# Kernel optimization log

Hardware: AMD Instinct MI355X
Metric: run time of the kernel (lower is better)

Reference implementation:

```python
import jax, jax.numpy as jnp
import numpy as np

N = 4096
IN_SIZE = 512
MLP_W = 16
HID = 512
MID = 64  # hardcoded tgc2 output size in the torch module
OUT = 128
BN_EPS = 1e-5


def setup_inputs() -> dict:
    key = jax.random.key(0)
    ks = jax.random.split(key, 24)
    adj = (jax.random.uniform(ks[0], (N, N)) < 0.05).astype(jnp.float32)
    xdeg = jax.random.uniform(ks[1], (N, N), dtype=jnp.float32)
    ydeg = jax.random.uniform(ks[2], (N, N), dtype=jnp.float32)
    u = lambda k, sh, fan: jax.random.uniform(k, sh, jnp.float32, -1.0, 1.0) / np.sqrt(fan)
    return {
        "adj": adj, "xdeg": xdeg, "ydeg": ydeg,
        # edge MLP: 3 -> MLP_W -> 2
        "mlp_w1": u(ks[3], (3, MLP_W), 3), "mlp_b1": jnp.zeros((MLP_W,), jnp.float32),
        "mlp_w2": u(ks[4], (MLP_W, 2), MLP_W), "mlp_b2": jnp.zeros((2,), jnp.float32),
        # positional linear: Linear(N, in_size) applied to eye(N) -> pe = W^T + b
        "pe_w": u(ks[5], (N, IN_SIZE), N), "pe_b": jnp.zeros((IN_SIZE,), jnp.float32),
        # GCN weights
        "gc1_w": u(ks[6], (IN_SIZE, HID), HID),
        "lin2_w": u(ks[7], (HID, MID), HID), "lin2_b": jnp.zeros((MID,), jnp.float32),
        "gc3_w": u(ks[8], (MID, OUT), OUT),
        # BatchNorm (eval mode: running stats)
        "bn1_g": jnp.ones((HID,), jnp.float32), "bn1_b": jnp.zeros((HID,), jnp.float32),
        "bn1_m": jnp.zeros((HID,), jnp.float32), "bn1_v": jnp.ones((HID,), jnp.float32),
        "bn2_g": jnp.ones((OUT,), jnp.float32), "bn2_b": jnp.zeros((OUT,), jnp.float32),
        "bn2_m": jnp.zeros((OUT,), jnp.float32), "bn2_v": jnp.ones((OUT,), jnp.float32),
    }


def reference(adj, xdeg, ydeg, mlp_w1, mlp_b1, mlp_w2, mlp_b2, pe_w, pe_b,
              gc1_w, lin2_w, lin2_b, gc3_w,
              bn1_g, bn1_b, bn1_m, bn1_v, bn2_g, bn2_b, bn2_m, bn2_v):
    # Edge MLP + softmax over [adj, xdeg, ydeg] features; torch only computes it
    # at nonzero adj entries then scatters into a dense mask. Since the mask is
    # multiplied by adj, computing densely and multiplying is exactly equivalent.
    feats = jnp.stack([adj, xdeg, ydeg], axis=-1)          # [N, N, 3]
    h = jax.nn.relu(jnp.einsum('nmf,fw->nmw', feats, mlp_w1) + mlp_b1)
    logits = jnp.einsum('nmw,wc->nmc', h, mlp_w2) + mlp_b2  # [N, N, 2]
    mask = jax.nn.softmax(logits, axis=-1)[..., 1]          # [N, N]
    a = adj * mask + jnp.eye(adj.shape[0], dtype=adj.dtype)

    # Degree normalization: A' = D_row^{-1/2} A D_col^{-1/2} (broadcast, no diag matmuls)
    rowsum = jnp.sum(a, axis=1)
    colsum = jnp.sum(a, axis=0)
    d_row = jnp.where(rowsum > 0, rowsum ** -0.5, 0.0)
    d_col = jnp.where(colsum > 0, colsum ** -0.5, 0.0)
    a = d_row[:, None] * a * d_col[None, :]

    # pe = Linear(eye(N)) = W^T + b (eval mode, dropout off)
    pe = pe_w + pe_b[None, :]                               # [N, IN_SIZE]

    h = a @ (pe @ gc1_w)                                    # GCN layer 1
    h = (h - bn1_m) * (bn1_g / jnp.sqrt(bn1_v + BN_EPS)) + bn1_b
    h = h @ lin2_w + lin2_b                                 # tgc2
    mid = h
    h = jax.nn.relu(h)
    h = a @ (h @ gc3_w)                                     # GCN layer 3
    out = (h - bn2_m) * (bn2_g / jnp.sqrt(bn2_v + BN_EPS)) + bn2_b
    return out, mid
```

## Files before the change

### kernel.cpp

```cpp
#include <hip/hip_runtime.h>
#include <hip/hip_bf16.h>

#define NN 4096
#define INS 512
#define HIDW 512
#define MIDW 64
#define OUTW 128
#define CAP 384
#define SEG 96
#define BN_EPS 1e-5f
#define CS_BLOCKS 256
#define CS_ROWS (NN / CS_BLOCKS)
#define NSTRIP 8

__global__ __launch_bounds__(256) void k_count(
    const float* __restrict__ adj,
    unsigned long long* __restrict__ msk, int* __restrict__ cnt,
    int* __restrict__ dflag)
{
    const int t = threadIdx.x;
    const int wave = t >> 6, lane = t & 63;
    const int gw = blockIdx.x * 4 + wave;
    const int i = gw >> 3, s = gw & 7;
    const int colbase = s * 512;
    const float* __restrict__ base = adj + (size_t)i * NN + colbase + 4 * lane;
    float4 a4a = *reinterpret_cast<const float4*>(base);
    float4 a4b = *reinterpret_cast<const float4*>(base + 256);
    const float av[8] = {a4a.x, a4a.y, a4a.z, a4a.w,
                         a4b.x, a4b.y, a4b.z, a4b.w};
    unsigned long long m[8];
    int total = 0;
    #pragma unroll
    for (int c = 0; c < 8; ++c) {
        int col = colbase + ((c < 4) ? (4 * lane + c) : (256 + 4 * lane + c - 4));
        bool diag = (col == i);
        bool act = (av[c] != 0.f) || diag;
        if (diag) dflag[i] = (av[c] != 0.f) ? 1 : 0;
        m[c] = __ballot(act);
        total += __popcll(m[c]);
    }
    if (lane == 0) {
        unsigned long long* mp = msk + (size_t)gw * 8;
        #pragma unroll
        for (int c = 0; c < 8; ++c) mp[c] = m[c];
        cnt[gw] = total;
    }
}

__global__ __launch_bounds__(256) void k_prefix(
    const int* __restrict__ cnt, int* __restrict__ off, int* __restrict__ nnz)
{
    int i = blockIdx.x * 256 + threadIdx.x;
    int run = 0;
    #pragma unroll
    for (int s = 0; s < NSTRIP; ++s) {
        off[i * NSTRIP + s] = run;
        run += cnt[i * NSTRIP + s];
    }
    nnz[i] = (run < CAP) ? run : CAP;
}

__global__ __launch_bounds__(256) void k_fill(
    const float* __restrict__ xdeg, const float* __restrict__ ydeg,
    const unsigned long long* __restrict__ msk, const int* __restrict__ off,
    const int* __restrict__ dflag,
    const float* __restrict__ w1, const float* __restrict__ b1,
    const float* __restrict__ w2, const float* __restrict__ b2,
    float* __restrict__ a_vals, int* __restrict__ a_cols,
    float* __restrict__ rs_part)
{
    __shared__ float shb[16], sw1x[16], sw1y[16], sw2[32], sb2[2];
    __shared__ int   scol[4][SEG];
    __shared__ float sx[4][SEG];
    __shared__ float sy[4][SEG];
    const int t = threadIdx.x;
    const int wave = t >> 6, lane = t & 63;
    if (t < 16) {
        shb[t]  = b1[t] + w1[t];
        sw1x[t] = w1[16 + t];
        sw1y[t] = w1[32 + t];
    }
    if (t < 32) sw2[t] = w2[t];
    if (t < 2)  sb2[t] = b2[t];
    __syncthreads();

    const int gw = __builtin_amdgcn_readfirstlane(blockIdx.x * 4 + wave);
    const int i = gw >> 3, s = gw & 7;
    const int colbase = s * 512;
    const size_t rbase = (size_t)i * NN + colbase + 4 * lane;
    float4 x4a = *reinterpret_cast<const float4*>(xdeg + rbase);
    float4 x4b = *reinterpret_cast<const float4*>(xdeg + rbase + 256);
    float4 y4a = *reinterpret_cast<const float4*>(ydeg + rbase);
    float4 y4b = *reinterpret_cast<const float4*>(ydeg + rbase + 256);
    const unsigned long long* __restrict__ mp = msk + (size_t)gw * 8;
    unsigned long long mm[8];
    #pragma unroll
    for (int c = 0; c < 8; ++c) mm[c] = mp[c];
    const int wb = off[gw];
    const int hasde = dflag[i];

    int bases[8];
    bases[0] = 0;
    #pragma unroll
    for (int c = 1; c < 8; ++c) bases[c] = bases[c - 1] + __popcll(mm[c - 1]);
    const int cnt_ = bases[7] + __popcll(mm[7]);
    const int n = (cnt_ < SEG) ? cnt_ : SEG;
    const unsigned long long lt = (1ULL << lane) - 1ULL;

    const float xv[8] = {x4a.x, x4a.y, x4a.z, x4a.w,
                         x4b.x, x4b.y, x4b.z, x4b.w};
    const float yv[8] = {y4a.x, y4a.y, y4a.z, y4a.w,
                         y4b.x, y4b.y, y4b.z, y4b.w};
    #pragma unroll
    for (int c = 0; c < 8; ++c) {
        if ((mm[c] >> lane) & 1ULL) {
            int pos = bases[c] + __popcll(mm[c] & lt);
            if (pos < SEG) {
                scol[wave][pos] = colbase + ((c < 4) ? (4 * lane + c)
                                                     : (256 + 4 * lane + c - 4));
                sx[wave][pos] = xv[c];
                sy[wave][pos] = yv[c];
            }
        }
    }

    float* __restrict__ gv = a_vals + (size_t)i * CAP;
    int*   __restrict__ gc = a_cols + (size_t)i * CAP;
    float local = 0.f;
    for (int p = lane; p < n; p += 64) {
        int col = scol[wave][p];
        float x = sx[wave][p], y = sy[wave][p];
        float l0 = sb2[0], l1 = sb2[1];
        #pragma unroll
        for (int w = 0; w < 16; ++w) {
            float hw = fmaf(x, sw1x[w], shb[w]);
            hw = fmaf(y, sw1y[w], hw);
            hw = fmaxf(hw, 0.f);
            l0 = fmaf(hw, sw2[2 * w],     l0);
            l1 = fmaf(hw, sw2[2 * w + 1], l1);
        }
        float v = 1.f / (1.f + __expf(l0 - l1));
        if (col == i) v = hasde ? (v + 1.f) : 1.f;
        int gp = wb + p;
        if (gp < CAP) { gc[gp] = col; gv[gp] = v; }
        local += v;
    }
    #pragma unroll
    for (int o = 32; o >= 1; o >>= 1)
        local += __shfl_down(local, o, 64);
    if (lane == 0) rs_part[gw] = local;
}

__global__ __launch_bounds__(256) void k_colsum(
    const float* __restrict__ a_vals, const int* __restrict__ a_cols,
    const int* __restrict__ nnz, float* __restrict__ P)
{
    __shared__ float ls[NN];
    const int t = threadIdx.x;
    const int b = blockIdx.x;
    for (int j = t; j < NN; j += 256) ls[j] = 0.f;
    __syncthreads();
    const int r0 = b * CS_ROWS;
    for (int r = r0; r < r0 + CS_ROWS; ++r) {
        const int n = nnz[r];
        const float* __restrict__ vr = a_vals + (size_t)r * CAP;
        const int*   __restrict__ cr = a_cols + (size_t)r * CAP;
        for (int p = t; p < n; p += 256)
            atomicAdd(&ls[cr[p]], vr[p]);
    }
    __syncthreads();
    for (int j = t; j < NN; j += 256)
        P[(size_t)b * NN + j] = ls[j];
}

__global__ __launch_bounds__(512) void k_misc(
    const float* __restrict__ lin2_w, const float* __restrict__ lin2_b,
    const float* __restrict__ bn1_g, const float* __restrict__ bn1_b,
    const float* __restrict__ bn1_m, const float* __restrict__ bn1_v,
    const float* __restrict__ bn2_g, const float* __restrict__ bn2_b,
    const float* __restrict__ bn2_m, const float* __restrict__ bn2_v,
    const float* __restrict__ rs_part, const float* __restrict__ P,
    float* __restrict__ Wp, float* __restrict__ c1,
    float* __restrict__ s2g, float* __restrict__ t2g,
    float* __restrict__ d_row, float* __restrict__ d_col)
{
    const int t = threadIdx.x;
    if (blockIdx.x == 0) {
        __shared__ float t1s[HIDW];
        {
            int h = t;
            float s1 = bn1_g[h] * rsqrtf(bn1_v[h] + BN_EPS);
            t1s[h] = bn1_b[h] - bn1_m[h] * s1;
            for (int m = 0; m < MIDW; ++m)
                Wp[(size_t)h * MIDW + m] = s1 * lin2_w[(size_t)h * MIDW + m];
        }
        __syncthreads();
        if (t < MIDW) {
            float acc = lin2_b[t];
            for (int h = 0; h < HIDW; ++h)
                acc = fmaf(t1s[h], lin2_w[(size_t)h * MIDW + t], acc);
            c1[t] = acc;
        } else if (t >= 64 && t < 64 + OUTW) {
            int j = t - 64;
            float s2 = bn2_g[j] * rsqrtf(bn2_v[j] + BN_EPS);
            s2g[j] = s2;
            t2g[j] = bn2_b[j] - bn2_m[j] * s2;
        }
    } else {
        int j = (blockIdx.x - 1) * 512 + t;
        float r = 0.f;
        #pragma unroll
        for (int s = 0; s < NSTRIP; ++s) r += rs_part[j * NSTRIP + s];
        d_row[j] = (r > 0.f) ? 1.f / sqrtf(r) : 0.f;
        float c = 0.f;
        for (int b = 0; b < CS_BLOCKS; ++b)
            c += P[(size_t)b * NN + j];
        d_col[j] = (c > 0.f) ? 1.f / sqrtf(c) : 0.f;
    }
}

template <bool ABIAS, bool ROWSCALE>
__global__ __launch_bounds__(256) void k_thin(
    const float* __restrict__ A, const float* __restrict__ B,
    const float* __restrict__ abias, const float* __restrict__ rscale,
    float* __restrict__ C, int M, int K)
{
    __shared__ float As[64][36];
    __shared__ float Bs[64][64];
    const int t = threadIdx.x;
    const int bm = blockIdx.x * 32;
    const int c2 = t & 31, rg = t >> 5;

    float acc[4][2] = {};

    for (int k0 = 0; k0 < K; k0 += 64) {
        #pragma unroll
        for (int l = 0; l < 8; ++l) {
            int e = t + l * 256;
            int r = e >> 6, k = e & 63;
            float v = A[(size_t)(bm + r) * K + k0 + k];
            if (ABIAS) v += abias[k0 + k];
            As[k][r] = v;
        }
        #pragma unroll
        for (int l = 0; l < 16; ++l) {
            int e = t + l * 256;
            int k = e >> 6, n = e & 63;
            Bs[k][n] = B[(size_t)(k0 + k) * 64 + n];
        }
        __syncthreads();
        #pragma unroll
        for (int k = 0; k < 64; ++k) {
            float4 a4 = *reinterpret_cast<const float4*>(&As[k][rg * 4]);
            float2 b2 = *reinterpret_cast<const float2*>(&Bs[k][2 * c2]);
            acc[0][0] = fmaf(a4.x, b2.x, acc[0][0]);
            acc[0][1] = fmaf(a4.x, b2.y, acc[0][1]);
            acc[1][0] = fmaf(a4.y, b2.x, acc[1][0]);
            acc[1][1] = fmaf(a4.y, b2.y, acc[1][1]);
            acc[2][0] = fmaf(a4.z, b2.x, acc[2][0]);
            acc[2][1] = fmaf(a4.z, b2.y, acc[2][1]);
            acc[3][0] = fmaf(a4.w, b2.x, acc[3][0]);
            acc[3][1] = fmaf(a4.w, b2.y, acc[3][1]);
        }
        __syncthreads();
    }

    #pragma unroll
    for (int u = 0; u < 4; ++u) {
        int r = bm + rg * 4 + u;
        float sc = ROWSCALE ? rscale[r] : 1.f;
        float2 o = make_float2(acc[u][0] * sc, acc[u][1] * sc);
        *reinterpret_cast<float2*>(&C[(size_t)r * 64 + 2 * c2]) = o;
    }
}

template <bool WITH_MID>
__global__ __launch_bounds__(256) void k_spmm(
    const float* __restrict__ a_vals, const int* __restrict__ a_cols,
    const int* __restrict__ nnz, const float* __restrict__ X,
    const float* __restrict__ d_row, const float* __restrict__ d_col,
    const float* __restrict__ c1,
    float* __restrict__ O1, float* __restrict__ O2)
{
    __shared__ float sv[2][CAP];
    __shared__ int   scl[2][CAP];
    __shared__ float sacc[4][64];
    const int t = threadIdx.x;
    const int wave = t >> 6, lane = t & 63;
    const int rb = wave >> 1, h = wave & 1;
    const int i = blockIdx.x * 2 + rb;
    const int n = nnz[i];
    const int n16 = (n + 15) & ~15;
    const float* __restrict__ vrow = a_vals + (size_t)i * CAP;
    const int*   __restrict__ crow = a_cols + (size_t)i * CAP;

    for (int p = h * 64 + lane; p < n16; p += 128) {
        bool ok = p < n;
        sv[rb][p]  = ok ? vrow[p] : 0.f;
        scl[rb][p] = ok ? crow[p] : 0;
    }
    __syncthreads();

    const int eh = lane >> 5;
    const int lc = lane & 31;
    const int Q  = n16 >> 1;
    const int Qh = Q >> 1;

    float a0 = 0.f, a1 = 0.f;
    for (int q = h * Qh; q < (h + 1) * Qh; q += 4) {
        #pragma unroll
        for (int j = 0; j < 4; ++j) {
            int p = 2 * (q + j) + eh;
            float v = sv[rb][p];
            int c = scl[rb][p];
            float2 x = *reinterpret_cast<const float2*>(X + (size_t)c * 64 + 2 * lc);
            a0 = fmaf(v, x.x, a0);
            a1 = fmaf(v, x.y, a1);
        }
    }
    a0 += __shfl_xor(a0, 32);
    a1 += __shfl_xor(a1, 32);
    if (lane < 32) { sacc[wave][2 * lc] = a0; sacc[wave][2 * lc + 1] = a1; }
    __syncthreads();

    if (h == 0 && lane < 32) {
        float s0 = sacc[wave][2 * lc]     + sacc[wave + 1][2 * lc];
        float s1 = sacc[wave][2 * lc + 1] + sacc[wave + 1][2 * lc + 1];
        float dr = d_row[i];
        if (WITH_MID) {
            float dc = d_col[i];
            float m0 = fmaf(s0, dr, c1[2 * lc]);
            float m1 = fmaf(s1, dr, c1[2 * lc + 1]);
            *reinterpret_cast<float2*>(O1 + (size_t)i * 64 + 2 * lc) =
                make_float2(m0, m1);
            *reinterpret_cast<float2*>(O2 + (size_t)i * 64 + 2 * lc) =
                make_float2(dc * fmaxf(m0, 0.f), dc * fmaxf(m1, 0.f));
        } else {
            *reinterpret_cast<float2*>(O1 + (size_t)i * 64 + 2 * lc) =
                make_float2(s0 * dr, s1 * dr);
        }
    }
}

__global__ __launch_bounds__(256) void k_out(
    const float* __restrict__ S, const float* __restrict__ gc3,
    const float* __restrict__ s2g, const float* __restrict__ t2g,
    float* __restrict__ out)
{
    __shared__ float Ss[64][20];
    __shared__ float Gs[64][128];
    const int t = threadIdx.x;
    const int bm = blockIdx.x * 16;

    {
        int r = t >> 4, c4 = (t & 15) * 4;
        float4 v = *reinterpret_cast<const float4*>(S + (size_t)(bm + r) * 64 + c4);
        Ss[c4 + 0][r] = v.x; Ss[c4 + 1][r] = v.y;
        Ss[c4 + 2][r] = v.z; Ss[c4 + 3][r] = v.w;
    }
    #pragma unroll
    for (int l = 0; l < 32; ++l) {
        int e = t + l * 256;
        Gs[e >> 7][e & 127] = gc3[e];
    }
    __syncthreads();

    const int j = t & 127;
    const int r0 = (t >> 7) * 8;
    float acc[8] = {};
    #pragma unroll
    for (int k = 0; k < 64; ++k) {
        float g = Gs[k][j];
        float4 a = *reinterpret_cast<const float4*>(&Ss[k][r0]);
        float4 b = *reinterpret_cast<const float4*>(&Ss[k][r0 + 4]);
        acc[0] = fmaf(a.x, g, acc[0]); acc[1] = fmaf(a.y, g, acc[1]);
        acc[2] = fmaf(a.z, g, acc[2]); acc[3] = fmaf(a.w, g, acc[3]);
        acc[4] = fmaf(b.x, g, acc[4]); acc[5] = fmaf(b.y, g, acc[5]);
        acc[6] = fmaf(b.z, g, acc[6]); acc[7] = fmaf(b.w, g, acc[7]);
    }
    float s2 = s2g[j], t2 = t2g[j];
    #pragma unroll
    for (int u = 0; u < 8; ++u)
        out[(size_t)(bm + r0 + u) * 128 + j] = fmaf(acc[u], s2, t2);
}

extern "C" void kernel_launch(void* const* d_in, const int* in_sizes, int n_in,
                              void* d_out, int out_size, void* d_ws, size_t ws_size,
                              hipStream_t stream) {
    const float* adj    = (const float*)d_in[0];
    const float* xdeg   = (const float*)d_in[1];
    const float* ydeg   = (const float*)d_in[2];
    const float* mlp_w1 = (const float*)d_in[3];
    const float* mlp_b1 = (const float*)d_in[4];
    const float* mlp_w2 = (const float*)d_in[5];
    const float* mlp_b2 = (const float*)d_in[6];
    const float* pe_w   = (const float*)d_in[7];
    const float* pe_b   = (const float*)d_in[8];
    const float* gc1_w  = (const float*)d_in[9];
    const float* lin2_w = (const float*)d_in[10];
    const float* lin2_b = (const float*)d_in[11];
    const float* gc3_w  = (const float*)d_in[12];
    const float* bn1_g  = (const float*)d_in[13];
    const float* bn1_b  = (const float*)d_in[14];
    const float* bn1_m  = (const float*)d_in[15];
    const float* bn1_v  = (const float*)d_in[16];
    const float* bn2_g  = (const float*)d_in[17];
    const float* bn2_b  = (const float*)d_in[18];
    const float* bn2_m  = (const float*)d_in[19];
    const float* bn2_v  = (const float*)d_in[20];

    float* out = (float*)d_out;
    float* mid = out + (size_t)NN * OUTW;

    char* w = (char*)d_ws;
    float* a_vals = (float*)w;  w += (size_t)NN * CAP * 4;
    int*   a_cols = (int*)w;    w += (size_t)NN * CAP * 4;
    int*   nnz    = (int*)w;    w += (size_t)NN * 4;
    unsigned long long* msk = (unsigned long long*)w; w += (size_t)NN * NSTRIP * 8 * 8;
    int*   cnt    = (int*)w;    w += (size_t)NN * NSTRIP * 4;
    int*   off    = (int*)w;    w += (size_t)NN * NSTRIP * 4;
    int*   dflag  = (int*)w;    w += (size_t)NN * 4;
    float* rs_part= (float*)w;  w += (size_t)NN * NSTRIP * 4;
    float* d_row  = (float*)w;  w += (size_t)NN * 4;
    float* d_col  = (float*)w;  w += (size_t)NN * 4;
    float* P      = (float*)w;  w += (size_t)CS_BLOCKS * NN * 4;
    float* Wp     = (float*)w;  w += (size_t)HIDW * MIDW * 4;
    float* W2     = (float*)w;  w += (size_t)INS * MIDW * 4;
    float* c1     = (float*)w;  w += 256;
    float* s2g    = (float*)w;  w += 512;
    float* t2g    = (float*)w;  w += 512;
    float* G      = (float*)w;  w += (size_t)NN * MIDW * 4;
    float* R      = (float*)w;  w += (size_t)NN * MIDW * 4;
    float* S      = (float*)w;  w += (size_t)NN * MIDW * 4;

    k_count<<<NN * NSTRIP / 4, 256, 0, stream>>>(adj, msk, cnt, dflag);
    k_prefix<<<NN / 256, 256, 0, stream>>>(cnt, off, nnz);
    k_fill<<<NN * NSTRIP / 4, 256, 0, stream>>>(
        xdeg, ydeg, msk, off, dflag, mlp_w1, mlp_b1, mlp_w2, mlp_b2,
        a_vals, a_cols, rs_part);
    k_colsum<<<CS_BLOCKS, 256, 0, stream>>>(a_vals, a_cols, nnz, P);
    k_misc<<<9, 512, 0, stream>>>(lin2_w, lin2_b, bn1_g, bn1_b, bn1_m, bn1_v,
                                  bn2_g, bn2_b, bn2_m, bn2_v, rs_part, P,
                                  Wp, c1, s2g, t2g, d_row, d_col);
    k_thin<false, false><<<INS / 32, 256, 0, stream>>>(
        gc1_w, Wp, nullptr, nullptr, W2, INS, HIDW);
    k_thin<true, true><<<NN / 32, 256, 0, stream>>>(
        pe_w, W2, pe_b, d_col, G, NN, INS);
    k_spmm<true><<<NN / 2, 256, 0, stream>>>(
        a_vals, a_cols, nnz, G, d_row, d_col, c1, mid, R);
    k_spmm<false><<<NN / 2, 256, 0, stream>>>(
        a_vals, a_cols, nnz, R, d_row, d_col, nullptr, S, nullptr);
    k_out<<<NN / 16, 256, 0, stream>>>(S, gc3_w, s2g, t2g, out);
}
```

Baseline: 136.9 us.

## Drop prefix kernel and fuse output GEMM into second SpMM

Removes the k_prefix launch. Each consumer now recomputes its row offset and nnz by summing the eight per-strip counts. Also fuses the final 64x128 gc3 projection and BatchNorm into the second SpMM's epilogue, which removes the k_out launch and the S intermediate round trip. This cuts two launches and some global traffic, at the cost of redundant count reads and a per-block gc3 read from global memory without LDS staging.

```diff
diff --git a/kernel.cpp b/kernel.cpp
--- a/kernel.cpp
+++ b/kernel.cpp
@@ -47,22 +47,9 @@
     }
 }
 
-__global__ __launch_bounds__(256) void k_prefix(
-    const int* __restrict__ cnt, int* __restrict__ off, int* __restrict__ nnz)
-{
-    int i = blockIdx.x * 256 + threadIdx.x;
-    int run = 0;
-    #pragma unroll
-    for (int s = 0; s < NSTRIP; ++s) {
-        off[i * NSTRIP + s] = run;
-        run += cnt[i * NSTRIP + s];
-    }
-    nnz[i] = (run < CAP) ? run : CAP;
-}
-
 __global__ __launch_bounds__(256) void k_fill(
     const float* __restrict__ xdeg, const float* __restrict__ ydeg,
-    const unsigned long long* __restrict__ msk, const int* __restrict__ off,
+    const unsigned long long* __restrict__ msk, const int* __restrict__ cnt,
     const int* __restrict__ dflag,
     const float* __restrict__ w1, const float* __restrict__ b1,
     const float* __restrict__ w2, const float* __restrict__ b2,
@@ -96,7 +83,10 @@
     unsigned long long mm[8];
     #pragma unroll
     for (int c = 0; c < 8; ++c) mm[c] = mp[c];
-    const int wb = off[gw];
+    const int* __restrict__ cb = cnt + i * NSTRIP;
+    int wb = 0;
+    #pragma unroll
+    for (int ss = 0; ss < NSTRIP; ++ss) if (ss < s) wb += cb[ss];
     const int hasde = dflag[i];
 
     int bases[8];
@@ -153,7 +143,7 @@
 
 __global__ __launch_bounds__(256) void k_colsum(
     const float* __restrict__ a_vals, const int* __restrict__ a_cols,
-    const int* __restrict__ nnz, float* __restrict__ P)
+    const int* __restrict__ cnt, float* __restrict__ P)
 {
     __shared__ float ls[NN];
     const int t = threadIdx.x;
@@ -162,7 +152,10 @@
     __syncthreads();
     const int r0 = b * CS_ROWS;
     for (int r = r0; r < r0 + CS_ROWS; ++r) {
-        const int n = nnz[r];
+        int n = 0;
+        #pragma unroll
+        for (int ss = 0; ss < NSTRIP; ++ss) n += cnt[r * NSTRIP + ss];
+        n = (n < CAP) ? n : CAP;
         const float* __restrict__ vr = a_vals + (size_t)r * CAP;
         const int*   __restrict__ cr = a_cols + (size_t)r * CAP;
         for (int p = t; p < n; p += 256)
@@ -277,9 +270,11 @@
 template <bool WITH_MID>
 __global__ __launch_bounds__(256) void k_spmm(
     const float* __restrict__ a_vals, const int* __restrict__ a_cols,
-    const int* __restrict__ nnz, const float* __restrict__ X,
+    const int* __restrict__ cnt, const float* __restrict__ X,
     const float* __restrict__ d_row, const float* __restrict__ d_col,
     const float* __restrict__ c1,
+    const float* __restrict__ gc3, const float* __restrict__ s2g,
+    const float* __restrict__ t2g,
     float* __restrict__ O1, float* __restrict__ O2)
 {
     __shared__ float sv[2][CAP];
@@ -289,7 +284,10 @@
     const int wave = t >> 6, lane = t & 63;
     const int rb = wave >> 1, h = wave & 1;
     const int i = blockIdx.x * 2 + rb;
-    const int n = nnz[i];
+    int n = 0;
+    #pragma unroll
+    for (int ss = 0; ss < NSTRIP; ++ss) n += cnt[i * NSTRIP + ss];
+    n = (n < CAP) ? n : CAP;
     const int n16 = (n + 15) & ~15;
     const float* __restrict__ vrow = a_vals + (size_t)i * CAP;
     const int*   __restrict__ crow = a_cols + (size_t)i * CAP;
@@ -323,11 +321,11 @@
     if (lane < 32) { sacc[wave][2 * lc] = a0; sacc[wave][2 * lc + 1] = a1; }
     __syncthreads();
 
-    if (h == 0 && lane < 32) {
-        float s0 = sacc[wave][2 * lc]     + sacc[wave + 1][2 * lc];
-        float s1 = sacc[wave][2 * lc + 1] + sacc[wave + 1][2 * lc + 1];
-        float dr = d_row[i];
-        if (WITH_MID) {
+    if (WITH_MID) {
+        if (h == 0 && lane < 32) {
+            float s0 = sacc[wave][2 * lc]     + sacc[wave + 1][2 * lc];
+            float s1 = sacc[wave][2 * lc + 1] + sacc[wave + 1][2 * lc + 1];
+            float dr = d_row[i];
             float dc = d_col[i];
             float m0 = fmaf(s0, dr, c1[2 * lc]);
             float m1 = fmaf(s1, dr, c1[2 * lc + 1]);
@@ -335,53 +333,26 @@
                 make_float2(m0, m1);
             *reinterpret_cast<float2*>(O2 + (size_t)i * 64 + 2 * lc) =
                 make_float2(dc * fmaxf(m0, 0.f), dc * fmaxf(m1, 0.f));
-        } else {
-            *reinterpret_cast<float2*>(O1 + (size_t)i * 64 + 2 * lc) =
-                make_float2(s0 * dr, s1 * dr);
-        }
-    }
-}
-
-__global__ __launch_bounds__(256) void k_out(
-    const float* __restrict__ S, const float* __restrict__ gc3,
-    const float* __restrict__ s2g, const float* __restrict__ t2g,
-    float* __restrict__ out)
-{
-    __shared__ float Ss[64][20];
-    __shared__ float Gs[64][128];
-    const int t = threadIdx.x;
-    const int bm = blockIdx.x * 16;
-
-    {
-        int r = t >> 4, c4 = (t & 15) * 4;
-        float4 v = *reinterpret_cast<const float4*>(S + (size_t)(bm + r) * 64 + c4);
-        Ss[c4 + 0][r] = v.x; Ss[c4 + 1][r] = v.y;
-        Ss[c4 + 2][r] = v.z; Ss[c4 + 3][r] = v.w;
-    }
-    #pragma unroll
-    for (int l = 0; l < 32; ++l) {
-        int e = t + l * 256;
-        Gs[e >> 7][e & 127] = gc3[e];
-    }
-    __syncthreads();
-
-    const int j = t & 127;
-    const int r0 = (t >> 7) * 8;
-    float acc[8] = {};
-    #pragma unroll
-    for (int k = 0; k < 64; ++k) {
-        float g = Gs[k][j];
-        float4 a = *reinterpret_cast<const float4*>(&Ss[k][r0]);
-        float4 b = *reinterpret_cast<const float4*>(&Ss[k][r0 + 4]);
-        acc[0] = fmaf(a.x, g, acc[0]); acc[1] = fmaf(a.y, g, acc[1]);
-        acc[2] = fmaf(a.z, g, acc[2]); acc[3] = fmaf(a.w, g, acc[3]);
-        acc[4] = fmaf(b.x, g, acc[4]); acc[5] = fmaf(b.y, g, acc[5]);
-        acc[6] = fmaf(b.z, g, acc[6]); acc[7] = fmaf(b.w, g, acc[7]);
-    }
-    float s2 = s2g[j], t2 = t2g[j];
-    #pragma unroll
-    for (int u = 0; u < 8; ++u)
-        out[(size_t)(bm + r0 + u) * 128 + j] = fmaf(acc[u], s2, t2);
+        }
+    } else {
+        if (h == 0 && lane < 32) {
+            float dr = d_row[i];
+            float s0 = (sacc[wave][2 * lc]     + sacc[wave + 1][2 * lc])     * dr;
+            float s1 = (sacc[wave][2 * lc + 1] + sacc[wave + 1][2 * lc + 1]) * dr;
+            sacc[wave][2 * lc]     = s0;
+            sacc[wave][2 * lc + 1] = s1;
+        }
+        __syncthreads();
+        const int rb2 = t >> 7;
+        const int j = t & 127;
+        const float* __restrict__ srow = sacc[2 * rb2];
+        float acc = 0.f;
+        #pragma unroll 8
+        for (int k = 0; k < 64; ++k)
+            acc = fmaf(srow[k], gc3[k * 128 + j], acc);
+        int orow = blockIdx.x * 2 + rb2;
+        O1[(size_t)orow * 128 + j] = fmaf(acc, s2g[j], t2g[j]);
+    }
 }
 
 extern "C" void kernel_launch(void* const* d_in, const int* in_sizes, int n_in,
@@ -415,10 +386,8 @@
     char* w = (char*)d_ws;
     float* a_vals = (float*)w;  w += (size_t)NN * CAP * 4;
     int*   a_cols = (int*)w;    w += (size_t)NN * CAP * 4;
-    int*   nnz    = (int*)w;    w += (size_t)NN * 4;
     unsigned long long* msk = (unsigned long long*)w; w += (size_t)NN * NSTRIP * 8 * 8;
     int*   cnt    = (int*)w;    w += (size_t)NN * NSTRIP * 4;
-    int*   off    = (int*)w;    w += (size_t)NN * NSTRIP * 4;
     int*   dflag  = (int*)w;    w += (size_t)NN * 4;
     float* rs_part= (float*)w;  w += (size_t)NN * NSTRIP * 4;
     float* d_row  = (float*)w;  w += (size_t)NN * 4;
@@ -431,14 +400,12 @@
     float* t2g    = (float*)w;  w += 512;
     float* G      = (float*)w;  w += (size_t)NN * MIDW * 4;
     float* R      = (float*)w;  w += (size_t)NN * MIDW * 4;
-    float* S      = (float*)w;  w += (size_t)NN * MIDW * 4;
 
     k_count<<<NN * NSTRIP / 4, 256, 0, stream>>>(adj, msk, cnt, dflag);
-    k_prefix<<<NN / 256, 256, 0, stream>>>(cnt, off, nnz);
     k_fill<<<NN * NSTRIP / 4, 256, 0, stream>>>(
-        xdeg, ydeg, msk, off, dflag, mlp_w1, mlp_b1, mlp_w2, mlp_b2,
+        xdeg, ydeg, msk, cnt, dflag, mlp_w1, mlp_b1, mlp_w2, mlp_b2,
         a_vals, a_cols, rs_part);
-    k_colsum<<<CS_BLOCKS, 256, 0, stream>>>(a_vals, a_cols, nnz, P);
+    k_colsum<<<CS_BLOCKS, 256, 0, stream>>>(a_vals, a_cols, cnt, P);
     k_misc<<<9, 512, 0, stream>>>(lin2_w, lin2_b, bn1_g, bn1_b, bn1_m, bn1_v,
                                   bn2_g, bn2_b, bn2_m, bn2_v, rs_part, P,
                                   Wp, c1, s2g, t2g, d_row, d_col);
@@ -447,8 +414,9 @@
     k_thin<true, true><<<NN / 32, 256, 0, stream>>>(
         pe_w, W2, pe_b, d_col, G, NN, INS);
     k_spmm<true><<<NN / 2, 256, 0, stream>>>(
-        a_vals, a_cols, nnz, G, d_row, d_col, c1, mid, R);
+        a_vals, a_cols, cnt, G, d_row, d_col, c1,
+        nullptr, nullptr, nullptr, mid, R);
     k_spmm<false><<<NN / 2, 256, 0, stream>>>(
-        a_vals, a_cols, nnz, R, d_row, d_col, nullptr, S, nullptr);
-    k_out<<<NN / 16, 256, 0, stream>>>(S, gc3_w, s2g, t2g, out);
-}
+        a_vals, a_cols, cnt, R, d_row, d_col, nullptr,
+        gc3_w, s2g, t2g, out, nullptr);
+}
```

New measurement: 135.9 us. About the same (-0.8%).
